# Kernel optimization log

Measured on AMD Instinct MI355X. Metric: run time of the kernel, lower is better.

The kernel has to match this reference:

```python
import jax, jax.numpy as jnp
import numpy as np

M, K, N = 8192, 4096, 4096

def setup_inputs() -> dict:
    key = jax.random.key(0)
    k0, k1, k2, k3, k4 = jax.random.split(key, 5)
    x = jax.random.normal(k0, (M, K), dtype=jnp.float32)
    # int8 weight stored as int32 spec dtype; values in [-127, 127]
    weight = jax.random.randint(k1, (N, K), -127, 128, dtype=jnp.int32)
    input_scale = jnp.array([0.02], dtype=jnp.float32)
    input_offset = jnp.zeros((1,), dtype=jnp.int32)
    # per-output-channel dequant scale (small positive)
    deq_scale = jax.random.uniform(k2, (N,), dtype=jnp.float32, minval=1e-4, maxval=2e-4)
    quant_bias = jax.random.randint(k3, (N,), -100, 101, dtype=jnp.int32)
    # sparse-compression output-channel reorder index (a permutation)
    index = jax.random.permutation(k4, N).astype(jnp.int32)
    return {"x": x, "weight": weight, "input_scale": input_scale,
            "input_offset": input_offset, "deq_scale": deq_scale,
            "quant_bias": quant_bias, "index": index}

def reference(x, weight, input_scale, input_offset, deq_scale, quant_bias, index):
    # 1) per-tensor activation quantization to int8
    x_q = jnp.clip(jnp.round(x / input_scale) + input_offset.astype(jnp.float32),
                   -128.0, 127.0).astype(jnp.int8)
    acc = jnp.matmul(x_q.astype(jnp.int32), weight.astype(jnp.int8).astype(jnp.int32).T)
    acc = acc + quant_bias  # [M, N] int32
    # 3) per-channel dequantization
    y = acc.astype(jnp.float32) * deq_scale  # [M, N]
    # 4) restore output-channel order from compressed layout
    return jnp.take(y, index, axis=-1)
```

## Files before the change

kernel.cpp:

```cpp
#include <hip/hip_runtime.h>
#include <hip/hip_bf16.h>
#include <stdint.h>

#define M_DIM 8192
#define K_DIM 4096
#define N_DIM 4096

#define BM 256
#define BN 256
#define BKB 64
#define NT (K_DIM / BKB)
#define ATILE (BM * BKB)
#define BTILE (BN * BKB)

typedef int i32x4 __attribute__((ext_vector_type(4)));

__global__ __launch_bounds__(256) void quant_x_kernel(
    const float* __restrict__ x, const float* __restrict__ scale_p,
    const int* __restrict__ off_p, int8_t* __restrict__ xq)
{
    const float s = scale_p[0];
    const float off = (float)off_p[0];
    long base = ((long)blockIdx.x * 256 + threadIdx.x) * 16;
    const float4* xin = (const float4*)(x + base);
    float v[16];
    *(float4*)(v + 0)  = xin[0];
    *(float4*)(v + 4)  = xin[1];
    *(float4*)(v + 8)  = xin[2];
    *(float4*)(v + 12) = xin[3];
    uint32_t pk[4];
#pragma unroll
    for (int g = 0; g < 4; ++g) {
        uint32_t p = 0;
#pragma unroll
        for (int j = 0; j < 4; ++j) {
            float q = rintf(v[g * 4 + j] / s) + off;
            q = fminf(fmaxf(q, -128.0f), 127.0f);
            int qi = (int)q;
            p |= ((uint32_t)(qi & 0xff)) << (8 * j);
        }
        pk[g] = p;
    }
    uint4 o; o.x = pk[0]; o.y = pk[1]; o.z = pk[2]; o.w = pk[3];
    *(uint4*)(xq + base) = o;
}

__global__ __launch_bounds__(256) void pack_w_kernel(
    const int* __restrict__ w, const int* __restrict__ index,
    const float* __restrict__ deq, const int* __restrict__ qb,
    int8_t* __restrict__ bp, float* __restrict__ dsp, int* __restrict__ qbp)
{
    int j = blockIdx.x;
    int t = threadIdx.x;
    int src = index[j];
    const int4* wrow = (const int4*)(w + (long)src * K_DIM);
    uint32_t pk[4];
#pragma unroll
    for (int g = 0; g < 4; ++g) {
        int4 c = wrow[t * 4 + g];
        pk[g] = ((uint32_t)(c.x & 0xff)) | (((uint32_t)(c.y & 0xff)) << 8) |
                (((uint32_t)(c.z & 0xff)) << 16) | (((uint32_t)(c.w & 0xff)) << 24);
    }
    uint4 o; o.x = pk[0]; o.y = pk[1]; o.z = pk[2]; o.w = pk[3];
    *(uint4*)(bp + (long)j * K_DIM + t * 16) = o;
    if (t == 0) { dsp[j] = deq[src]; qbp[j] = qb[src]; }
}

__device__ __forceinline__ void gload_lds16(const int8_t* g, int8_t* l)
{
    __builtin_amdgcn_global_load_lds(
        (const __attribute__((address_space(1))) uint32_t*)g,
        (__attribute__((address_space(3))) uint32_t*)l, 16, 0, 0);
}

__global__ __launch_bounds__(512, 2) void gemm_i8_kernel(
    const int8_t* __restrict__ A, const int8_t* __restrict__ B,
    const float* __restrict__ dsp, const int* __restrict__ qbp,
    float* __restrict__ C)
{
    __shared__ int8_t lds[3][ATILE + BTILE];

    int bid = blockIdx.x;
    int swz = (bid & 7) * (gridDim.x >> 3) + (bid >> 3);
    int bm = swz & 31;
    int bn = swz >> 5;
    int brow = bm * BM, bcol = bn * BN;

    int t = threadIdx.x;
    int wv = t >> 6;
    int l  = t & 63;
    int lr = l & 15;
    int ls = l >> 4;
    int wrM = (wv >> 2) * 128;
    int wcN = (wv & 3) * 64;
    int pslot = ls ^ ((lr >> 1) & 3);

    int aoff[8], boff[4];
#pragma unroll
    for (int m = 0; m < 8; ++m)
        aoff[m] = (wrM + m * 16 + lr) * BKB + pslot * 16;
#pragma unroll
    for (int n = 0; n < 4; ++n)
        boff[n] = ATILE + (wcN + n * 16 + lr) * BKB + pslot * 16;

    const int8_t* sa[2]; int da[2];
    const int8_t* sb[2]; int db[2];
#pragma unroll
    for (int i = 0; i < 2; ++i) {
        int ca = i * 512 + t;
        int row = ca >> 2;
        int lg = (ca & 3) ^ ((row >> 1) & 3);
        sa[i] = A + (long)(brow + row) * K_DIM + lg * 16;
        da[i] = ca * 16;
        sb[i] = B + (long)(bcol + row) * K_DIM + lg * 16;
        db[i] = ATILE + ca * 16;
    }

#pragma unroll
    for (int p = 0; p < 2; ++p) {
        gload_lds16(sa[0], &lds[p][da[0]]);
        gload_lds16(sa[1], &lds[p][da[1]]);
        gload_lds16(sb[0], &lds[p][db[0]]);
        gload_lds16(sb[1], &lds[p][db[1]]);
        sa[0] += BKB; sa[1] += BKB; sb[0] += BKB; sb[1] += BKB;
    }
    asm volatile("s_waitcnt vmcnt(4)" ::: "memory");
    __builtin_amdgcn_s_barrier();

    i32x4 acc[8][4] = {};
    int cur = 0, stg = 2;

    for (int kt = 0; kt < NT; ++kt) {
        const bool do_stage = (kt + 2) < NT;
        const int8_t* base = lds[cur];

        i32x4 af[8], bf[4];
#pragma unroll
        for (int n = 0; n < 4; ++n) bf[n] = *(const i32x4*)(base + boff[n]);
#pragma unroll
        for (int m = 0; m < 8; ++m) af[m] = *(const i32x4*)(base + aoff[m]);
        if (do_stage) {
            int8_t* sdst = lds[stg];
            gload_lds16(sa[0], sdst + da[0]);
            gload_lds16(sa[1], sdst + da[1]);
            gload_lds16(sb[0], sdst + db[0]);
            gload_lds16(sb[1], sdst + db[1]);
            sa[0] += BKB; sa[1] += BKB; sb[0] += BKB; sb[1] += BKB;
        }
        asm volatile("s_waitcnt lgkmcnt(0)" ::: "memory");
        __builtin_amdgcn_sched_barrier(0);
        __builtin_amdgcn_s_setprio(1);
#pragma unroll
        for (int m = 0; m < 8; ++m)
#pragma unroll
            for (int n = 0; n < 4; ++n)
                acc[m][n] = __builtin_amdgcn_mfma_i32_16x16x64_i8(
                    af[m], bf[n], acc[m][n], 0, 0, 0);
        __builtin_amdgcn_s_setprio(0);
        __builtin_amdgcn_sched_barrier(0);
        if (do_stage) asm volatile("s_waitcnt vmcnt(4)" ::: "memory");
        else          asm volatile("s_waitcnt vmcnt(0)" ::: "memory");
        __builtin_amdgcn_s_barrier();
        cur = (cur == 2) ? 0 : cur + 1;
        stg = (stg == 2) ? 0 : stg + 1;
    }

#pragma unroll
    for (int n = 0; n < 4; ++n) {
        int gc = bcol + wcN + n * 16 + lr;
        float ds = dsp[gc];
        int qb = qbp[gc];
#pragma unroll
        for (int m = 0; m < 8; ++m) {
            int gr0 = brow + wrM + m * 16 + ls * 4;
#pragma unroll
            for (int r = 0; r < 4; ++r) {
                C[(long)(gr0 + r) * N_DIM + gc] = (float)(acc[m][n][r] + qb) * ds;
            }
        }
    }
}

extern "C" void kernel_launch(void* const* d_in, const int* in_sizes, int n_in,
                              void* d_out, int out_size, void* d_ws, size_t ws_size,
                              hipStream_t stream)
{
    (void)in_sizes; (void)n_in; (void)out_size; (void)ws_size;
    const float* x   = (const float*)d_in[0];
    const int*   w   = (const int*)d_in[1];
    const float* is  = (const float*)d_in[2];
    const int*   io  = (const int*)d_in[3];
    const float* dq  = (const float*)d_in[4];
    const int*   qb  = (const int*)d_in[5];
    const int*   idx = (const int*)d_in[6];
    float* out = (float*)d_out;

    int8_t* xq  = (int8_t*)d_ws;
    int8_t* bp  = xq + (size_t)M_DIM * K_DIM;
    float*  dsp = (float*)(bp + (size_t)N_DIM * K_DIM);
    int*    qbp = (int*)(dsp + N_DIM);

    long quant_blocks = ((long)M_DIM * K_DIM) / 16 / 256;
    quant_x_kernel<<<(int)quant_blocks, 256, 0, stream>>>(x, is, io, xq);
    pack_w_kernel<<<N_DIM, 256, 0, stream>>>(w, idx, dq, qb, bp, dsp, qbp);
    gemm_i8_kernel<<<(M_DIM / BM) * (N_DIM / BN), 512, 0, stream>>>(xq, bp, dsp, qbp, out);
}
```

Before: 197.2 us.

## Use a four-stage LDS ring with register double-buffered fragments in the int8 GEMM

The GEMM main loop moves from a 3-buffer LDS pipeline to a 4-buffer ring. It keeps two register sets of A/B fragments, so LDS reads for the next K-tile are issued before the MFMAs of the current tile. The explicit lgkmcnt(0) wait before the MFMAs is removed. The loop is manually unrolled by four with a peeled tail, and address offsets are folded into constants. The aim is to hide LDS read latency behind MFMA work. The cost is 128KB of LDS per block and extra fragment registers, which risks spills under the 512x2 launch bounds.

```diff
diff --git a/kernel.cpp b/kernel.cpp
--- a/kernel.cpp
+++ b/kernel.cpp
@@ -11,7 +11,7 @@
 #define BKB 64
 #define NT (K_DIM / BKB)
 #define ATILE (BM * BKB)
-#define BTILE (BN * BKB)
+#define TBYTES (ATILE + BN * BKB)
 
 typedef int i32x4 __attribute__((ext_vector_type(4)));
 
@@ -78,7 +78,7 @@
     const float* __restrict__ dsp, const int* __restrict__ qbp,
     float* __restrict__ C)
 {
-    __shared__ int8_t lds[3][ATILE + BTILE];
+    __shared__ int8_t lds[4][TBYTES];
 
     int bid = blockIdx.x;
     int swz = (bid & 7) * (gridDim.x >> 3) + (bid >> 3);
@@ -95,75 +95,96 @@
     int wcN = (wv & 3) * 64;
     int pslot = ls ^ ((lr >> 1) & 3);
 
-    int aoff[8], boff[4];
-#pragma unroll
-    for (int m = 0; m < 8; ++m)
-        aoff[m] = (wrM + m * 16 + lr) * BKB + pslot * 16;
-#pragma unroll
-    for (int n = 0; n < 4; ++n)
-        boff[n] = ATILE + (wcN + n * 16 + lr) * BKB + pslot * 16;
-
-    const int8_t* sa[2]; int da[2];
-    const int8_t* sb[2]; int db[2];
-#pragma unroll
-    for (int i = 0; i < 2; ++i) {
-        int ca = i * 512 + t;
-        int row = ca >> 2;
-        int lg = (ca & 3) ^ ((row >> 1) & 3);
-        sa[i] = A + (long)(brow + row) * K_DIM + lg * 16;
-        da[i] = ca * 16;
-        sb[i] = B + (long)(bcol + row) * K_DIM + lg * 16;
-        db[i] = ATILE + ca * 16;
-    }
-
-#pragma unroll
-    for (int p = 0; p < 2; ++p) {
-        gload_lds16(sa[0], &lds[p][da[0]]);
-        gload_lds16(sa[1], &lds[p][da[1]]);
-        gload_lds16(sb[0], &lds[p][db[0]]);
-        gload_lds16(sb[1], &lds[p][db[1]]);
-        sa[0] += BKB; sa[1] += BKB; sb[0] += BKB; sb[1] += BKB;
-    }
+    const int aL = (wrM + lr) * BKB + pslot * 16;
+    const int bL = ATILE + (wcN + lr) * BKB + pslot * 16;
+
+    int ca0 = t, ca1 = 512 + t;
+    int r0 = ca0 >> 2, r1 = ca1 >> 2;
+    const int8_t* sa0 = A + (long)(brow + r0) * K_DIM + ((ca0 & 3) ^ ((r0 >> 1) & 3)) * 16;
+    const int8_t* sa1 = A + (long)(brow + r1) * K_DIM + ((ca1 & 3) ^ ((r1 >> 1) & 3)) * 16;
+    const int8_t* sb0 = B + (long)(bcol + r0) * K_DIM + ((ca0 & 3) ^ ((r0 >> 1) & 3)) * 16;
+    const int8_t* sb1 = B + (long)(bcol + r1) * K_DIM + ((ca1 & 3) ^ ((r1 >> 1) & 3)) * 16;
+    const int da0 = ca0 * 16, da1 = ca1 * 16;
+    const int db0 = ATILE + ca0 * 16, db1 = ATILE + ca1 * 16;
+
+#define STAGE(SBUF) do { \
+        int8_t* _d = &lds[SBUF][0]; \
+        gload_lds16(sa0, _d + da0); \
+        gload_lds16(sa1, _d + da1); \
+        gload_lds16(sb0, _d + db0); \
+        gload_lds16(sb1, _d + db1); \
+        sa0 += BKB; sa1 += BKB; sb0 += BKB; sb1 += BKB; \
+    } while (0)
+
+#define FRAG_READ(AF, BF, RBUF) do { \
+        const int8_t* _b = &lds[RBUF][0]; \
+        _Pragma("unroll") \
+        for (int n = 0; n < 4; ++n) BF[n] = *(const i32x4*)(_b + bL + n * 1024); \
+        _Pragma("unroll") \
+        for (int m = 0; m < 8; ++m) AF[m] = *(const i32x4*)(_b + aL + m * 1024); \
+    } while (0)
+
+#define MFMA32(AF, BF) do { \
+        __builtin_amdgcn_s_setprio(1); \
+        _Pragma("unroll") \
+        for (int m = 0; m < 8; ++m) \
+        _Pragma("unroll") \
+        for (int n = 0; n < 4; ++n) \
+            acc[m][n] = __builtin_amdgcn_mfma_i32_16x16x64_i8(AF[m], BF[n], acc[m][n], 0, 0, 0); \
+        __builtin_amdgcn_s_setprio(0); \
+    } while (0)
+
+#define TILE_END(VMC) do { \
+        __builtin_amdgcn_sched_barrier(0); \
+        asm volatile("s_waitcnt vmcnt(" #VMC ")" ::: "memory"); \
+        asm volatile("s_barrier" ::: "memory"); \
+    } while (0)
+
+    STAGE(0); STAGE(1); STAGE(2);
     asm volatile("s_waitcnt vmcnt(4)" ::: "memory");
-    __builtin_amdgcn_s_barrier();
-
+    asm volatile("s_barrier" ::: "memory");
+
+    i32x4 afA[8], bfA[4], afB[8], bfB[4];
     i32x4 acc[8][4] = {};
-    int cur = 0, stg = 2;
-
-    for (int kt = 0; kt < NT; ++kt) {
-        const bool do_stage = (kt + 2) < NT;
-        const int8_t* base = lds[cur];
-
-        i32x4 af[8], bf[4];
-#pragma unroll
-        for (int n = 0; n < 4; ++n) bf[n] = *(const i32x4*)(base + boff[n]);
-#pragma unroll
-        for (int m = 0; m < 8; ++m) af[m] = *(const i32x4*)(base + aoff[m]);
-        if (do_stage) {
-            int8_t* sdst = lds[stg];
-            gload_lds16(sa[0], sdst + da[0]);
-            gload_lds16(sa[1], sdst + da[1]);
-            gload_lds16(sb[0], sdst + db[0]);
-            gload_lds16(sb[1], sdst + db[1]);
-            sa[0] += BKB; sa[1] += BKB; sb[0] += BKB; sb[1] += BKB;
-        }
-        asm volatile("s_waitcnt lgkmcnt(0)" ::: "memory");
-        __builtin_amdgcn_sched_barrier(0);
-        __builtin_amdgcn_s_setprio(1);
-#pragma unroll
-        for (int m = 0; m < 8; ++m)
-#pragma unroll
-            for (int n = 0; n < 4; ++n)
-                acc[m][n] = __builtin_amdgcn_mfma_i32_16x16x64_i8(
-                    af[m], bf[n], acc[m][n], 0, 0, 0);
-        __builtin_amdgcn_s_setprio(0);
-        __builtin_amdgcn_sched_barrier(0);
-        if (do_stage) asm volatile("s_waitcnt vmcnt(4)" ::: "memory");
-        else          asm volatile("s_waitcnt vmcnt(0)" ::: "memory");
-        __builtin_amdgcn_s_barrier();
-        cur = (cur == 2) ? 0 : cur + 1;
-        stg = (stg == 2) ? 0 : stg + 1;
-    }
+
+    FRAG_READ(afA, bfA, 0);
+
+    for (int it = 0; it < 15; ++it) {
+        FRAG_READ(afB, bfB, 1); STAGE(3);
+        __builtin_amdgcn_sched_barrier(0);
+        MFMA32(afA, bfA);
+        TILE_END(4);
+        FRAG_READ(afA, bfA, 2); STAGE(0);
+        __builtin_amdgcn_sched_barrier(0);
+        MFMA32(afB, bfB);
+        TILE_END(4);
+        FRAG_READ(afB, bfB, 3); STAGE(1);
+        __builtin_amdgcn_sched_barrier(0);
+        MFMA32(afA, bfA);
+        TILE_END(4);
+        FRAG_READ(afA, bfA, 0); STAGE(2);
+        __builtin_amdgcn_sched_barrier(0);
+        MFMA32(afB, bfB);
+        TILE_END(4);
+    }
+
+    FRAG_READ(afB, bfB, 1); STAGE(3);
+    __builtin_amdgcn_sched_barrier(0);
+    MFMA32(afA, bfA);
+    TILE_END(4);
+    FRAG_READ(afA, bfA, 2);
+    __builtin_amdgcn_sched_barrier(0);
+    MFMA32(afB, bfB);
+    TILE_END(0);
+    FRAG_READ(afB, bfB, 3);
+    __builtin_amdgcn_sched_barrier(0);
+    MFMA32(afA, bfA);
+    MFMA32(afB, bfB);
+
+#undef STAGE
+#undef FRAG_READ
+#undef MFMA32
+#undef TILE_END
 
 #pragma unroll
     for (int n = 0; n < 4; ++n) {
```

After: 206.4 us. 4.7% more time.

## Split GEMM main loop into four interleaved load/MFMA phases with barriers

Applied to the files above, without the earlier changes.

Restructures each K iteration of the int8 GEMM into four phases. Each phase issues a subset of the LDS fragment reads and one global-to-LDS prefetch, then runs 8 MFMAs, instead of loading everything before 32 MFMAs. The aim is to interleave memory traffic with matrix-core work in a ping-pong style so loads overlap compute better. It adds seven extra workgroup barriers per iteration, which could cost more synchronisation than the overlap gains.

```diff
diff --git a/kernel.cpp b/kernel.cpp
--- a/kernel.cpp
+++ b/kernel.cpp
@@ -11,7 +11,7 @@
 #define BKB 64
 #define NT (K_DIM / BKB)
 #define ATILE (BM * BKB)
-#define BTILE (BN * BKB)
+#define TBYTES (ATILE + BN * BKB)
 
 typedef int i32x4 __attribute__((ext_vector_type(4)));
 
@@ -78,7 +78,7 @@
     const float* __restrict__ dsp, const int* __restrict__ qbp,
     float* __restrict__ C)
 {
-    __shared__ int8_t lds[3][ATILE + BTILE];
+    __shared__ int8_t lds[3][TBYTES];
 
     int bid = blockIdx.x;
     int swz = (bid & 7) * (gridDim.x >> 3) + (bid >> 3);
@@ -103,26 +103,39 @@
     for (int n = 0; n < 4; ++n)
         boff[n] = ATILE + (wcN + n * 16 + lr) * BKB + pslot * 16;
 
-    const int8_t* sa[2]; int da[2];
-    const int8_t* sb[2]; int db[2];
-#pragma unroll
-    for (int i = 0; i < 2; ++i) {
-        int ca = i * 512 + t;
-        int row = ca >> 2;
-        int lg = (ca & 3) ^ ((row >> 1) & 3);
-        sa[i] = A + (long)(brow + row) * K_DIM + lg * 16;
-        da[i] = ca * 16;
-        sb[i] = B + (long)(bcol + row) * K_DIM + lg * 16;
-        db[i] = ATILE + ca * 16;
-    }
+    int ca0 = t, ca1 = 512 + t;
+    int r0 = ca0 >> 2, r1 = ca1 >> 2;
+    const int8_t* sa0 = A + (long)(brow + r0) * K_DIM + ((ca0 & 3) ^ ((r0 >> 1) & 3)) * 16;
+    const int8_t* sa1 = A + (long)(brow + r1) * K_DIM + ((ca1 & 3) ^ ((r1 >> 1) & 3)) * 16;
+    const int8_t* sb0 = B + (long)(bcol + r0) * K_DIM + ((ca0 & 3) ^ ((r0 >> 1) & 3)) * 16;
+    const int8_t* sb1 = B + (long)(bcol + r1) * K_DIM + ((ca1 & 3) ^ ((r1 >> 1) & 3)) * 16;
+    const int da0 = ca0 * 16, da1 = ca1 * 16;
+    const int db0 = ATILE + ca0 * 16, db1 = ATILE + ca1 * 16;
+
+#define LGKM0_FENCE() do { \
+        asm volatile("s_waitcnt lgkmcnt(0)" ::: "memory"); \
+        __builtin_amdgcn_sched_barrier(0); \
+    } while (0)
+
+#define MFMA8(MLO, NLO) do { \
+        __builtin_amdgcn_s_setprio(1); \
+        _Pragma("unroll") \
+        for (int m = 0; m < 4; ++m) \
+        _Pragma("unroll") \
+        for (int n = 0; n < 2; ++n) \
+            acc[(MLO) + m][(NLO) + n] = __builtin_amdgcn_mfma_i32_16x16x64_i8( \
+                af[(MLO) + m], bf[(NLO) + n], acc[(MLO) + m][(NLO) + n], 0, 0, 0); \
+        __builtin_amdgcn_s_setprio(0); \
+    } while (0)
 
 #pragma unroll
     for (int p = 0; p < 2; ++p) {
-        gload_lds16(sa[0], &lds[p][da[0]]);
-        gload_lds16(sa[1], &lds[p][da[1]]);
-        gload_lds16(sb[0], &lds[p][db[0]]);
-        gload_lds16(sb[1], &lds[p][db[1]]);
-        sa[0] += BKB; sa[1] += BKB; sb[0] += BKB; sb[1] += BKB;
+        int8_t* d = &lds[p][0];
+        gload_lds16(sa0, d + da0);
+        gload_lds16(sa1, d + da1);
+        gload_lds16(sb0, d + db0);
+        gload_lds16(sb1, d + db1);
+        sa0 += BKB; sa1 += BKB; sb0 += BKB; sb1 += BKB;
     }
     asm volatile("s_waitcnt vmcnt(4)" ::: "memory");
     __builtin_amdgcn_s_barrier();
@@ -133,37 +146,51 @@
     for (int kt = 0; kt < NT; ++kt) {
         const bool do_stage = (kt + 2) < NT;
         const int8_t* base = lds[cur];
+        int8_t* sdst = lds[stg];
 
         i32x4 af[8], bf[4];
-#pragma unroll
-        for (int n = 0; n < 4; ++n) bf[n] = *(const i32x4*)(base + boff[n]);
-#pragma unroll
-        for (int m = 0; m < 8; ++m) af[m] = *(const i32x4*)(base + aoff[m]);
-        if (do_stage) {
-            int8_t* sdst = lds[stg];
-            gload_lds16(sa[0], sdst + da[0]);
-            gload_lds16(sa[1], sdst + da[1]);
-            gload_lds16(sb[0], sdst + db[0]);
-            gload_lds16(sb[1], sdst + db[1]);
-            sa[0] += BKB; sa[1] += BKB; sb[0] += BKB; sb[1] += BKB;
-        }
-        asm volatile("s_waitcnt lgkmcnt(0)" ::: "memory");
+
+        bf[0] = *(const i32x4*)(base + boff[0]);
+        bf[1] = *(const i32x4*)(base + boff[1]);
+#pragma unroll
+        for (int m = 0; m < 4; ++m) af[m] = *(const i32x4*)(base + aoff[m]);
+        if (do_stage) { gload_lds16(sa0, sdst + da0); sa0 += BKB; }
+        __builtin_amdgcn_s_barrier();
+        LGKM0_FENCE();
+        MFMA8(0, 0);
+        __builtin_amdgcn_s_barrier();
+
+        bf[2] = *(const i32x4*)(base + boff[2]);
+        bf[3] = *(const i32x4*)(base + boff[3]);
+        if (do_stage) { gload_lds16(sa1, sdst + da1); sa1 += BKB; }
+        __builtin_amdgcn_s_barrier();
+        LGKM0_FENCE();
+        MFMA8(0, 2);
+        __builtin_amdgcn_s_barrier();
+
+#pragma unroll
+        for (int m = 4; m < 8; ++m) af[m] = *(const i32x4*)(base + aoff[m]);
+        if (do_stage) { gload_lds16(sb0, sdst + db0); sb0 += BKB; }
+        __builtin_amdgcn_s_barrier();
+        LGKM0_FENCE();
+        MFMA8(4, 0);
+        __builtin_amdgcn_s_barrier();
+
+        if (do_stage) { gload_lds16(sb1, sdst + db1); sb1 += BKB; }
+        __builtin_amdgcn_s_barrier();
         __builtin_amdgcn_sched_barrier(0);
-        __builtin_amdgcn_s_setprio(1);
-#pragma unroll
-        for (int m = 0; m < 8; ++m)
-#pragma unroll
-            for (int n = 0; n < 4; ++n)
-                acc[m][n] = __builtin_amdgcn_mfma_i32_16x16x64_i8(
-                    af[m], bf[n], acc[m][n], 0, 0, 0);
-        __builtin_amdgcn_s_setprio(0);
+        MFMA8(4, 2);
         __builtin_amdgcn_sched_barrier(0);
         if (do_stage) asm volatile("s_waitcnt vmcnt(4)" ::: "memory");
         else          asm volatile("s_waitcnt vmcnt(0)" ::: "memory");
         __builtin_amdgcn_s_barrier();
+
         cur = (cur == 2) ? 0 : cur + 1;
         stg = (stg == 2) ? 0 : stg + 1;
     }
+
+#undef LGKM0_FENCE
+#undef MFMA8
 
 #pragma unroll
     for (int n = 0; n < 4; ++n) {
```

After: 201.1 us. About the same (+2.0%).
